# Optimization experiments

Hardware: AMD Instinct MI355X
Metric: run time of the kernel (lower is better)

## Reference

```python
import jax, jax.numpy as jnp
import numpy as np

B, T, C = 4, 2048, 1024
H, DK, DV = 16, 64, 64


def setup_inputs() -> dict:
    key = jax.random.key(0)
    ks = jax.random.split(key, 12)
    s = 1.0 / np.sqrt(C)
    inp = {
        "Q": jax.random.normal(ks[0], (B, T, C), jnp.float32),
        "K": jax.random.normal(ks[1], (B, T, C), jnp.float32),
        "V": jax.random.normal(ks[2], (B, T, C), jnp.float32),
        # causal mask: True (==1) means masked out
        "mask": jnp.broadcast_to(jnp.triu(jnp.ones((T, T), bool), k=1), (B, 1, T, T)),
        "Wq": jax.random.uniform(ks[3], (C, H * DK), jnp.float32, -s, s),
        "bq": jax.random.uniform(ks[4], (H * DK,), jnp.float32, -s, s),
        "Wk": jax.random.uniform(ks[5], (C, H * DK), jnp.float32, -s, s),
        "bk": jax.random.uniform(ks[6], (H * DK,), jnp.float32, -s, s),
        "Wv": jax.random.uniform(ks[7], (C, H * DV), jnp.float32, -s, s),
        "bv": jax.random.uniform(ks[8], (H * DV,), jnp.float32, -s, s),
        "Wo": jax.random.uniform(ks[9], (H * DV, C), jnp.float32, -s, s),
        "bo": jax.random.uniform(ks[10], (C,), jnp.float32, -s, s),
    }
    return inp


def _split(x, d):
    b, t, _ = x.shape
    return x.reshape(b, t, H, d).transpose(0, 2, 1, 3)  # (B,H,T,d)


def reference(Q, K, V, mask, Wq, bq, Wk, bk, Wv, bv, Wo, bo):
    Qh = _split(Q @ Wq + bq, DK)
    Kh = _split(K @ Wk + bk, DK)
    Vh = _split(V @ Wv + bv, DV)
    scores = jnp.einsum('bhqd,bhkd->bhqk', Qh, Kh) / jnp.sqrt(jnp.float32(DK))
    scores = jnp.where(mask, -jnp.inf, scores)
    attn = jax.nn.softmax(scores, axis=-1)
    out = jnp.einsum('bhqk,bhkd->bhqd', attn, Vh)
    out = out.transpose(0, 2, 1, 3).reshape(B, T, H * DV)
    return out @ Wo + bo
```

## Files before the change

### kernel.cpp

```cpp
#include <hip/hip_runtime.h>
#include <stdint.h>

#define BATCH 4
#define SEQ   2048
#define CH    1024
#define NH    16
#define HD    64

#define QSCALE 0.18033688011112042f

#define GM 8192
#define GN 1024
#define GK 1024

typedef __attribute__((ext_vector_type(8))) short bf16x8;
typedef __attribute__((ext_vector_type(4))) short bf16x4;
typedef __attribute__((ext_vector_type(4))) float f32x4;

__device__ inline unsigned short f2bf(float f) {
    unsigned u = __float_as_uint(f);
    u += 0x7fff + ((u >> 16) & 1);
    return (unsigned short)(u >> 16);
}

__device__ inline float fast_exp2(float x) {
    float r;
    asm("v_exp_f32 %0, %1" : "=v"(r) : "v"(x));
    return r;
}

__device__ inline unsigned cvt_pk_bf16(float lo, float hi) {
    unsigned r;
    asm("v_cvt_pk_bf16_f32 %0, %1, %2" : "=v"(r) : "v"(lo), "v"(hi));
    return r;
}

#if __has_builtin(__builtin_amdgcn_mfma_f32_16x16x16bf16_1k)
__device__ inline void mfma16(f32x4& c, bf16x4 a, bf16x4 b) {
    c = __builtin_amdgcn_mfma_f32_16x16x16bf16_1k(a, b, c, 0, 0, 0);
}
#else
__device__ inline void mfma16(f32x4& c, bf16x4 a, bf16x4 b) {
    asm volatile("s_nop 2\n\tv_mfma_f32_16x16x16_bf16 %0, %1, %2, %0"
                 : "+v"(c) : "v"(a), "v"(b));
}
#endif

__device__ inline void gld_lds16(const void* g, void* l) {
    __builtin_amdgcn_global_load_lds((const __attribute__((address_space(1))) void*)g,
                                     (__attribute__((address_space(3))) void*)l,
                                     16, 0, 0);
}

__global__ __launch_bounds__(256) void prep_k(
    const float* __restrict__ Q, const float* __restrict__ K, const float* __restrict__ V,
    unsigned short* __restrict__ Qbf, unsigned short* __restrict__ Kbf, unsigned short* __restrict__ Vbf,
    const float* __restrict__ Wq, const float* __restrict__ Wk,
    const float* __restrict__ Wv, const float* __restrict__ Wo,
    unsigned short* __restrict__ WqT, unsigned short* __restrict__ WkT,
    unsigned short* __restrict__ WvT, unsigned short* __restrict__ WoT)
{
    const int bid = blockIdx.x;
    if (bid < 12288) {
        const int j     = bid >> 12;
        const int local = bid & 4095;
        const float* in = (j == 0) ? Q : (j == 1) ? K : V;
        unsigned short* out = (j == 0) ? Qbf : (j == 1) ? Kbf : Vbf;
        const int i = (local * 256 + threadIdx.x) * 8;
        f32x4 a = *(const f32x4*)(in + i);
        f32x4 b = *(const f32x4*)(in + i + 4);
        union { bf16x8 v; unsigned short s[8]; } o;
        o.s[0] = f2bf(a[0]); o.s[1] = f2bf(a[1]); o.s[2] = f2bf(a[2]); o.s[3] = f2bf(a[3]);
        o.s[4] = f2bf(b[0]); o.s[5] = f2bf(b[1]); o.s[6] = f2bf(b[2]); o.s[7] = f2bf(b[3]);
        *(bf16x8*)(out + i) = o.v;
    } else {
        __shared__ float tile[32][33];
        const int idx   = bid - 12288;
        const int j     = idx >> 10;
        const int local = idx & 1023;
        const float* W = (j == 0) ? Wq : (j == 1) ? Wk : (j == 2) ? Wv : Wo;
        unsigned short* Wt = (j == 0) ? WqT : (j == 1) ? WkT : (j == 2) ? WvT : WoT;
        const int bx = (local & 31) * 32;
        const int by = (local >> 5) * 32;
        const int tx = threadIdx.x & 31;
        const int ty = threadIdx.x >> 5;
#pragma unroll
        for (int i = 0; i < 32; i += 8)
            tile[ty + i][tx] = W[(size_t)(by + ty + i) * CH + bx + tx];
        __syncthreads();
#pragma unroll
        for (int i = 0; i < 32; i += 8)
            Wt[(size_t)(bx + ty + i) * CH + by + tx] = f2bf(tile[tx][ty + i]);
    }
}

__global__ __launch_bounds__(256, 2)
void qkv_gemm(const unsigned short* __restrict__ Qbf, const unsigned short* __restrict__ Kbf,
              const unsigned short* __restrict__ Vbf,
              const unsigned short* __restrict__ WqT, const unsigned short* __restrict__ WkT,
              const unsigned short* __restrict__ WvT,
              const float* __restrict__ bq, const float* __restrict__ bk,
              const float* __restrict__ bv,
              unsigned short* __restrict__ Qhb, unsigned short* __restrict__ Khb,
              unsigned short* __restrict__ Vtb)
{
    __shared__ unsigned short As[128 * 64];
    __shared__ unsigned short Bs[128 * 64];
    const int job = blockIdx.y;
    const unsigned short* A   = (job == 0) ? Qbf : (job == 1) ? Kbf : Vbf;
    const unsigned short* Bt  = (job == 0) ? WqT : (job == 1) ? WkT : WvT;
    const float* bias         = (job == 0) ? bq  : (job == 1) ? bk  : bv;
    unsigned short* outp      = (job == 0) ? Qhb : (job == 1) ? Khb : Vtb;
    const float oscale        = (job == 0) ? QSCALE : 1.0f;

    const int tid  = threadIdx.x;
    const int lane = tid & 63;
    const int w    = tid >> 6;
    const int nbn  = GN >> 7;
    const int nbm  = GM >> 7;
    const int xcd  = blockIdx.x & 7;
    const int idx  = blockIdx.x >> 3;
    const int mb   = xcd * (nbm >> 3) + idx / nbn;
    const int nb   = idx % nbn;
    const int m0   = mb << 7;
    const int n0   = nb << 7;
    const int wrow = (w >> 1) << 6;
    const int wcol = (w & 1) << 6;
    const int lr   = lane & 15;
    const int lg   = lane >> 4;

    f32x4 acc[4][4] = {};

    for (int k0 = 0; k0 < GK; k0 += 64) {
#pragma unroll
        for (int i = 0; i < 4; ++i) {
            int chunk = i * 256 + tid;
            int row = chunk >> 3;
            int c8  = (chunk & 7) << 3;
            gld_lds16(A  + (size_t)(m0 + row) * GK + k0 + c8, (char*)As + chunk * 16);
            gld_lds16(Bt + (size_t)(n0 + row) * GK + k0 + c8, (char*)Bs + chunk * 16);
        }
        __syncthreads();
#pragma unroll
        for (int kk = 0; kk < 2; ++kk) {
            bf16x8 af[4], bfr[4];
#pragma unroll
            for (int f = 0; f < 4; ++f)
                af[f] = *(const bf16x8*)(As + (wrow + f * 16 + lr) * 64 + kk * 32 + lg * 8);
#pragma unroll
            for (int f = 0; f < 4; ++f)
                bfr[f] = *(const bf16x8*)(Bs + (wcol + f * 16 + lr) * 64 + kk * 32 + lg * 8);
#pragma unroll
            for (int i = 0; i < 4; ++i)
#pragma unroll
                for (int j = 0; j < 4; ++j)
                    acc[i][j] = __builtin_amdgcn_mfma_f32_16x16x32_bf16(af[i], bfr[j], acc[i][j], 0, 0, 0);
        }
        __syncthreads();
    }

    float bvals[4];
#pragma unroll
    for (int j = 0; j < 4; ++j) bvals[j] = bias[n0 + wcol + j * 16 + lr];

    if (job < 2) {
#pragma unroll
        for (int i = 0; i < 4; ++i) {
            const int mbase = m0 + wrow + i * 16 + lg * 4;
#pragma unroll
            for (int j = 0; j < 4; ++j) {
                const int n = n0 + wcol + j * 16 + lr;
                const int h = n >> 6, d = n & 63;
#pragma unroll
                for (int r = 0; r < 4; ++r) {
                    const int m = mbase + r;
                    const int b = m >> 11, t = m & 2047;
                    outp[((size_t)(b * NH + h) * SEQ + t) * HD + d] = f2bf((acc[i][j][r] + bvals[j]) * oscale);
                }
            }
        }
    } else {
#pragma unroll
        for (int i = 0; i < 4; ++i) {
            const int mbase = m0 + wrow + i * 16 + lg * 4;
#pragma unroll
            for (int j = 0; j < 4; ++j) {
                const int n = n0 + wcol + j * 16 + lr;
                const int h = n >> 6, d = n & 63;
                const int b = mbase >> 11, t = mbase & 2047;
                union { unsigned short s[4]; uint2 v; } pk;
#pragma unroll
                for (int r = 0; r < 4; ++r) pk.s[r] = f2bf(acc[i][j][r] + bvals[j]);
                *(uint2*)(outp + ((size_t)(b * NH + h) * HD + d) * SEQ + t) = pk.v;
            }
        }
    }
}

__global__ __launch_bounds__(256, 2)
void gemm_out(const unsigned short* __restrict__ A,
              const unsigned short* __restrict__ Bt,
              const float* __restrict__ bias,
              float* __restrict__ out)
{
    __shared__ unsigned short As[128 * 64];
    __shared__ unsigned short Bs[128 * 64];
    const int tid  = threadIdx.x;
    const int lane = tid & 63;
    const int w    = tid >> 6;
    const int nbn  = GN >> 7;
    const int nbm  = GM >> 7;
    const int xcd  = blockIdx.x & 7;
    const int idx  = blockIdx.x >> 3;
    const int mb   = xcd * (nbm >> 3) + idx / nbn;
    const int nb   = idx % nbn;
    const int m0   = mb << 7;
    const int n0   = nb << 7;
    const int wrow = (w >> 1) << 6;
    const int wcol = (w & 1) << 6;
    const int lr   = lane & 15;
    const int lg   = lane >> 4;

    f32x4 acc[4][4] = {};

    for (int k0 = 0; k0 < GK; k0 += 64) {
#pragma unroll
        for (int i = 0; i < 4; ++i) {
            int chunk = i * 256 + tid;
            int row = chunk >> 3;
            int c8  = (chunk & 7) << 3;
            gld_lds16(A  + (size_t)(m0 + row) * GK + k0 + c8, (char*)As + chunk * 16);
            gld_lds16(Bt + (size_t)(n0 + row) * GK + k0 + c8, (char*)Bs + chunk * 16);
        }
        __syncthreads();
#pragma unroll
        for (int kk = 0; kk < 2; ++kk) {
            bf16x8 af[4], bfr[4];
#pragma unroll
            for (int f = 0; f < 4; ++f)
                af[f] = *(const bf16x8*)(As + (wrow + f * 16 + lr) * 64 + kk * 32 + lg * 8);
#pragma unroll
            for (int f = 0; f < 4; ++f)
                bfr[f] = *(const bf16x8*)(Bs + (wcol + f * 16 + lr) * 64 + kk * 32 + lg * 8);
#pragma unroll
            for (int i = 0; i < 4; ++i)
#pragma unroll
                for (int j = 0; j < 4; ++j)
                    acc[i][j] = __builtin_amdgcn_mfma_f32_16x16x32_bf16(af[i], bfr[j], acc[i][j], 0, 0, 0);
        }
        __syncthreads();
    }

    float bvals[4];
#pragma unroll
    for (int j = 0; j < 4; ++j) bvals[j] = bias[n0 + wcol + j * 16 + lr];

#pragma unroll
    for (int i = 0; i < 4; ++i) {
        const int mbase = m0 + wrow + i * 16 + lg * 4;
#pragma unroll
        for (int j = 0; j < 4; ++j) {
            const int n = n0 + wcol + j * 16 + lr;
#pragma unroll
            for (int r = 0; r < 4; ++r)
                out[(size_t)(mbase + r) * GN + n] = acc[i][j][r] + bvals[j];
        }
    }
}

__global__ __launch_bounds__(256, 4)
void attn_k(const unsigned short* __restrict__ Qh,
            const unsigned short* __restrict__ Kh,
            const unsigned short* __restrict__ Vt,
            unsigned short* __restrict__ O) {
    __shared__ unsigned short Ks[2][64 * 64];
    __shared__ unsigned short Vs[2][64 * 64];
    const int bh    = blockIdx.x;
    const int qtile = 31 - blockIdx.y;
    const int q0    = qtile << 6;
    const int tid  = threadIdx.x;
    const int lane = tid & 63;
    const int w    = tid >> 6;
    const int lr   = lane & 15;
    const int lg   = lane >> 4;
    const int qw   = q0 + w * 16;
    const int swz8 = (lr & 7) << 3;

    bf16x4 ones4;
#pragma unroll
    for (int j = 0; j < 4; ++j) ones4[j] = (short)0x3F80;

    bf16x8 qf[2];
#pragma unroll
    for (int kk = 0; kk < 2; ++kk)
        qf[kk] = *(const bf16x8*)(Qh + ((size_t)bh * SEQ + qw + lr) * HD + kk * 32 + lg * 8);

    float mrun = -3e38f;
    f32x4 ot[4] = {};
    f32x4 osum = {};

    const int nkt = qtile + 1;

#define STAGE(KT, B) do {                                                          \
        const int kv_ = (KT) << 6;                                                 \
        _Pragma("unroll")                                                          \
        for (int i_ = 0; i_ < 2; ++i_) {                                           \
            int c_ = i_ * 256 + tid;                                               \
            int row_ = c_ >> 3;                                                    \
            int so_ = (((c_ & 7) ^ (row_ & 7)) << 3);                              \
            gld_lds16(Kh + ((size_t)bh * SEQ + kv_ + row_) * HD + so_,             \
                      (char*)Ks[B] + c_ * 16);                                     \
            gld_lds16(Vt + ((size_t)bh * HD + row_) * SEQ + kv_ + so_,             \
                      (char*)Vs[B] + c_ * 16);                                     \
        }                                                                          \
    } while (0)

    STAGE(0, 0);
    __syncthreads();

    for (int kt = 0; kt < nkt; ++kt) {
        if (kt + 1 < nkt) STAGE(kt + 1, (kt + 1) & 1);
        const unsigned short* Kc = Ks[kt & 1];
        const unsigned short* Vc = Vs[kt & 1];
        const int kv0 = kt << 6;

        f32x4 s[4] = {};
#pragma unroll
        for (int kk = 0; kk < 2; ++kk) {
            const int u = (((kk << 2) | lg) ^ (lr & 7)) << 3;
#pragma unroll
            for (int f = 0; f < 4; ++f) {
                bf16x8 kb = *(const bf16x8*)(Kc + (f * 16 + lr) * 64 + u);
                s[f] = __builtin_amdgcn_mfma_f32_16x16x32_bf16(kb, qf[kk], s[f], 0, 0, 0);
            }
        }

        float rmax = -3e38f;
        if (kv0 + 63 <= qw) {
#pragma unroll
            for (int f = 0; f < 4; ++f)
#pragma unroll
                for (int r = 0; r < 4; ++r) rmax = fmaxf(rmax, s[f][r]);
        } else {
            const int q = qw + lr;
#pragma unroll
            for (int f = 0; f < 4; ++f)
#pragma unroll
                for (int r = 0; r < 4; ++r) {
                    const int kv = kv0 + f * 16 + lg * 4 + r;
                    float v = (kv > q) ? -3e38f : s[f][r];
                    s[f][r] = v;
                    rmax = fmaxf(rmax, v);
                }
        }
        rmax = fmaxf(rmax, __shfl_xor(rmax, 16));
        rmax = fmaxf(rmax, __shfl_xor(rmax, 32));

        if (__any(rmax > mrun)) {
            float mn = fmaxf(mrun, rmax);
            float c  = fast_exp2(mrun - mn);
            mrun = mn;
            osum *= c;
#pragma unroll
            for (int dd = 0; dd < 4; ++dd) ot[dd] *= c;
        }

#pragma unroll
        for (int f = 0; f < 4; ++f) {
#pragma unroll
            for (int r = 0; r < 4; ++r)
                s[f][r] = fast_exp2(s[f][r] - mrun);
            union { bf16x4 v; unsigned u[2]; } pb;
            pb.u[0] = cvt_pk_bf16(s[f][0], s[f][1]);
            pb.u[1] = cvt_pk_bf16(s[f][2], s[f][3]);
            mfma16(osum, ones4, pb.v);
#pragma unroll
            for (int dd = 0; dd < 4; ++dd) {
                bf16x4 va = *(const bf16x4*)(Vc + (dd * 16 + lr) * 64 + ((f * 16 + lg * 4) ^ swz8));
                mfma16(ot[dd], va, pb.v);
            }
        }
        __syncthreads();
    }
#undef STAGE

    const int b = bh >> 4, h = bh & 15;
    const float inv = 1.0f / osum[0];
    const int t = qw + lr;
#pragma unroll
    for (int dd = 0; dd < 4; ++dd) {
        union { unsigned short s4[4]; uint2 v; } pk;
#pragma unroll
        for (int r = 0; r < 4; ++r) pk.s4[r] = f2bf(ot[dd][r] * inv);
        *(uint2*)(O + ((size_t)b * SEQ + t) * CH + h * HD + dd * 16 + lg * 4) = pk.v;
    }
}

extern "C" void kernel_launch(void* const* d_in, const int* in_sizes, int n_in,
                              void* d_out, int out_size, void* d_ws, size_t ws_size,
                              hipStream_t stream) {
    const float* Q  = (const float*)d_in[0];
    const float* K  = (const float*)d_in[1];
    const float* V  = (const float*)d_in[2];
    const float* Wq = (const float*)d_in[4];
    const float* bq = (const float*)d_in[5];
    const float* Wk = (const float*)d_in[6];
    const float* bk = (const float*)d_in[7];
    const float* Wv = (const float*)d_in[8];
    const float* bv = (const float*)d_in[9];
    const float* Wo = (const float*)d_in[10];
    const float* bo = (const float*)d_in[11];
    float* out = (float*)d_out;

    const size_t SZ_ACT = (size_t)BATCH * SEQ * CH;
    const size_t SZ_W   = (size_t)CH * CH;

    char* p = (char*)d_ws;
    unsigned short* Qbf = (unsigned short*)p; p += SZ_ACT * 2;
    unsigned short* Kbf = (unsigned short*)p; p += SZ_ACT * 2;
    unsigned short* Vbf = (unsigned short*)p; p += SZ_ACT * 2;
    unsigned short* WqT = (unsigned short*)p; p += SZ_W * 2;
    unsigned short* WkT = (unsigned short*)p; p += SZ_W * 2;
    unsigned short* WvT = (unsigned short*)p; p += SZ_W * 2;
    unsigned short* WoT = (unsigned short*)p; p += SZ_W * 2;
    unsigned short* Qhb = (unsigned short*)p; p += SZ_ACT * 2;
    unsigned short* Khb = (unsigned short*)p; p += SZ_ACT * 2;
    unsigned short* Vtb = (unsigned short*)p; p += SZ_ACT * 2;
    unsigned short* Ob  = Qbf;

    prep_k<<<16384, 256, 0, stream>>>(Q, K, V, Qbf, Kbf, Vbf,
                                      Wq, Wk, Wv, Wo, WqT, WkT, WvT, WoT);

    qkv_gemm<<<dim3((GM / 128) * (GN / 128), 3), 256, 0, stream>>>(
        Qbf, Kbf, Vbf, WqT, WkT, WvT, bq, bk, bv, Qhb, Khb, Vtb);

    attn_k<<<dim3(BATCH * NH, SEQ / 64), 256, 0, stream>>>(Qhb, Khb, Vtb, Ob);

    gemm_out<<<(GM / 128) * (GN / 128), 256, 0, stream>>>(Ob, WoT, bo, out);
}
```

Before: 189.2 us.

## Fuse fp32-to-bf16 activation conversion into QKV GEMM loads; reswizzle V tile

Drops the separate pass that turned Q/K/V fp32 activations into bf16 buffers. The QKV GEMM now reads fp32 rows directly into registers, converts them with packed bf16 conversion and stores them to shared memory, while the weight tile still uses async global-to-LDS loads. This removes a full write and re-read of three activation tensors, at the cost of synchronous register-staged A loads with less latency hiding. Separately, the V tile swizzle in attention is changed to XOR on row pairs to reduce LDS bank conflicts for the 4-element V reads.

```diff
diff --git a/kernel.cpp b/kernel.cpp
--- a/kernel.cpp
+++ b/kernel.cpp
@@ -53,50 +53,32 @@
 }
 
 __global__ __launch_bounds__(256) void prep_k(
-    const float* __restrict__ Q, const float* __restrict__ K, const float* __restrict__ V,
-    unsigned short* __restrict__ Qbf, unsigned short* __restrict__ Kbf, unsigned short* __restrict__ Vbf,
     const float* __restrict__ Wq, const float* __restrict__ Wk,
     const float* __restrict__ Wv, const float* __restrict__ Wo,
     unsigned short* __restrict__ WqT, unsigned short* __restrict__ WkT,
     unsigned short* __restrict__ WvT, unsigned short* __restrict__ WoT)
 {
-    const int bid = blockIdx.x;
-    if (bid < 12288) {
-        const int j     = bid >> 12;
-        const int local = bid & 4095;
-        const float* in = (j == 0) ? Q : (j == 1) ? K : V;
-        unsigned short* out = (j == 0) ? Qbf : (j == 1) ? Kbf : Vbf;
-        const int i = (local * 256 + threadIdx.x) * 8;
-        f32x4 a = *(const f32x4*)(in + i);
-        f32x4 b = *(const f32x4*)(in + i + 4);
-        union { bf16x8 v; unsigned short s[8]; } o;
-        o.s[0] = f2bf(a[0]); o.s[1] = f2bf(a[1]); o.s[2] = f2bf(a[2]); o.s[3] = f2bf(a[3]);
-        o.s[4] = f2bf(b[0]); o.s[5] = f2bf(b[1]); o.s[6] = f2bf(b[2]); o.s[7] = f2bf(b[3]);
-        *(bf16x8*)(out + i) = o.v;
-    } else {
-        __shared__ float tile[32][33];
-        const int idx   = bid - 12288;
-        const int j     = idx >> 10;
-        const int local = idx & 1023;
-        const float* W = (j == 0) ? Wq : (j == 1) ? Wk : (j == 2) ? Wv : Wo;
-        unsigned short* Wt = (j == 0) ? WqT : (j == 1) ? WkT : (j == 2) ? WvT : WoT;
-        const int bx = (local & 31) * 32;
-        const int by = (local >> 5) * 32;
-        const int tx = threadIdx.x & 31;
-        const int ty = threadIdx.x >> 5;
-#pragma unroll
-        for (int i = 0; i < 32; i += 8)
-            tile[ty + i][tx] = W[(size_t)(by + ty + i) * CH + bx + tx];
-        __syncthreads();
-#pragma unroll
-        for (int i = 0; i < 32; i += 8)
-            Wt[(size_t)(bx + ty + i) * CH + by + tx] = f2bf(tile[tx][ty + i]);
-    }
+    __shared__ float tile[32][33];
+    const int j     = blockIdx.x >> 10;
+    const int local = blockIdx.x & 1023;
+    const float* W = (j == 0) ? Wq : (j == 1) ? Wk : (j == 2) ? Wv : Wo;
+    unsigned short* Wt = (j == 0) ? WqT : (j == 1) ? WkT : (j == 2) ? WvT : WoT;
+    const int bx = (local & 31) * 32;
+    const int by = (local >> 5) * 32;
+    const int tx = threadIdx.x & 31;
+    const int ty = threadIdx.x >> 5;
+#pragma unroll
+    for (int i = 0; i < 32; i += 8)
+        tile[ty + i][tx] = W[(size_t)(by + ty + i) * CH + bx + tx];
+    __syncthreads();
+#pragma unroll
+    for (int i = 0; i < 32; i += 8)
+        Wt[(size_t)(bx + ty + i) * CH + by + tx] = f2bf(tile[tx][ty + i]);
 }
 
 __global__ __launch_bounds__(256, 2)
-void qkv_gemm(const unsigned short* __restrict__ Qbf, const unsigned short* __restrict__ Kbf,
-              const unsigned short* __restrict__ Vbf,
+void qkv_gemm(const float* __restrict__ Qf, const float* __restrict__ Kf,
+              const float* __restrict__ Vf,
               const unsigned short* __restrict__ WqT, const unsigned short* __restrict__ WkT,
               const unsigned short* __restrict__ WvT,
               const float* __restrict__ bq, const float* __restrict__ bk,
@@ -107,7 +89,7 @@
     __shared__ unsigned short As[128 * 64];
     __shared__ unsigned short Bs[128 * 64];
     const int job = blockIdx.y;
-    const unsigned short* A   = (job == 0) ? Qbf : (job == 1) ? Kbf : Vbf;
+    const float* A32          = (job == 0) ? Qf  : (job == 1) ? Kf  : Vf;
     const unsigned short* Bt  = (job == 0) ? WqT : (job == 1) ? WkT : WvT;
     const float* bias         = (job == 0) ? bq  : (job == 1) ? bk  : bv;
     unsigned short* outp      = (job == 0) ? Qhb : (job == 1) ? Khb : Vtb;
@@ -132,13 +114,32 @@
     f32x4 acc[4][4] = {};
 
     for (int k0 = 0; k0 < GK; k0 += 64) {
+        f32x4 a0[4], a1[4];
 #pragma unroll
         for (int i = 0; i < 4; ++i) {
             int chunk = i * 256 + tid;
             int row = chunk >> 3;
             int c8  = (chunk & 7) << 3;
-            gld_lds16(A  + (size_t)(m0 + row) * GK + k0 + c8, (char*)As + chunk * 16);
+            const float* src = A32 + (size_t)(m0 + row) * GK + k0 + c8;
+            a0[i] = *(const f32x4*)src;
+            a1[i] = *(const f32x4*)(src + 4);
+        }
+#pragma unroll
+        for (int i = 0; i < 4; ++i) {
+            int chunk = i * 256 + tid;
+            int row = chunk >> 3;
+            int c8  = (chunk & 7) << 3;
             gld_lds16(Bt + (size_t)(n0 + row) * GK + k0 + c8, (char*)Bs + chunk * 16);
+        }
+#pragma unroll
+        for (int i = 0; i < 4; ++i) {
+            int chunk = i * 256 + tid;
+            union { bf16x8 v; unsigned u[4]; } wv;
+            wv.u[0] = cvt_pk_bf16(a0[i][0], a0[i][1]);
+            wv.u[1] = cvt_pk_bf16(a0[i][2], a0[i][3]);
+            wv.u[2] = cvt_pk_bf16(a1[i][0], a1[i][1]);
+            wv.u[3] = cvt_pk_bf16(a1[i][2], a1[i][3]);
+            *(bf16x8*)(As + chunk * 8) = wv.v;
         }
         __syncthreads();
 #pragma unroll
@@ -284,7 +285,6 @@
     const int lr   = lane & 15;
     const int lg   = lane >> 4;
     const int qw   = q0 + w * 16;
-    const int swz8 = (lr & 7) << 3;
 
     bf16x4 ones4;
 #pragma unroll
@@ -307,10 +307,11 @@
         for (int i_ = 0; i_ < 2; ++i_) {                                           \
             int c_ = i_ * 256 + tid;                                               \
             int row_ = c_ >> 3;                                                    \
-            int so_ = (((c_ & 7) ^ (row_ & 7)) << 3);                              \
-            gld_lds16(Kh + ((size_t)bh * SEQ + kv_ + row_) * HD + so_,             \
+            int sk_ = (((c_ & 7) ^ (row_ & 7)) << 3);                              \
+            int sv_ = (((c_ & 7) ^ ((row_ >> 1) & 7)) << 3);                       \
+            gld_lds16(Kh + ((size_t)bh * SEQ + kv_ + row_) * HD + sk_,             \
                       (char*)Ks[B] + c_ * 16);                                     \
-            gld_lds16(Vt + ((size_t)bh * HD + row_) * SEQ + kv_ + so_,             \
+            gld_lds16(Vt + ((size_t)bh * HD + row_) * SEQ + kv_ + sv_,             \
                       (char*)Vs[B] + c_ * 16);                                     \
         }                                                                          \
     } while (0)
@@ -376,7 +377,8 @@
             mfma16(osum, ones4, pb.v);
 #pragma unroll
             for (int dd = 0; dd < 4; ++dd) {
-                bf16x4 va = *(const bf16x4*)(Vc + (dd * 16 + lr) * 64 + ((f * 16 + lg * 4) ^ swz8));
+                const int vcol = ((((f << 1) | (lg >> 1)) ^ (lr >> 1)) << 3) | ((lg & 1) << 2);
+                bf16x4 va = *(const bf16x4*)(Vc + (dd * 16 + lr) * 64 + vcol);
                 mfma16(ot[dd], va, pb.v);
             }
         }
@@ -416,9 +418,6 @@
     const size_t SZ_W   = (size_t)CH * CH;
 
     char* p = (char*)d_ws;
-    unsigned short* Qbf = (unsigned short*)p; p += SZ_ACT * 2;
-    unsigned short* Kbf = (unsigned short*)p; p += SZ_ACT * 2;
-    unsigned short* Vbf = (unsigned short*)p; p += SZ_ACT * 2;
     unsigned short* WqT = (unsigned short*)p; p += SZ_W * 2;
     unsigned short* WkT = (unsigned short*)p; p += SZ_W * 2;
     unsigned short* WvT = (unsigned short*)p; p += SZ_W * 2;
@@ -426,13 +425,12 @@
     unsigned short* Qhb = (unsigned short*)p; p += SZ_ACT * 2;
     unsigned short* Khb = (unsigned short*)p; p += SZ_ACT * 2;
     unsigned short* Vtb = (unsigned short*)p; p += SZ_ACT * 2;
-    unsigned short* Ob  = Qbf;
-
-    prep_k<<<16384, 256, 0, stream>>>(Q, K, V, Qbf, Kbf, Vbf,
-                                      Wq, Wk, Wv, Wo, WqT, WkT, WvT, WoT);
+    unsigned short* Ob  = (unsigned short*)p; p += SZ_ACT * 2;
+
+    prep_k<<<4096, 256, 0, stream>>>(Wq, Wk, Wv, Wo, WqT, WkT, WvT, WoT);
 
     qkv_gemm<<<dim3((GM / 128) * (GN / 128), 3), 256, 0, stream>>>(
-        Qbf, Kbf, Vbf, WqT, WkT, WvT, bq, bk, bv, Qhb, Khb, Vtb);
+        Q, K, V, WqT, WkT, WvT, bq, bk, bv, Qhb, Khb, Vtb);
 
     attn_k<<<dim3(BATCH * NH, SEQ / 64), 256, 0, stream>>>(Qhb, Khb, Vtb, Ob);
 
```

New measurement: 185.5 us. 2.0% less time.
